# Optimization experiments

Measured on AMD Instinct MI355X. Metric: run time of the kernel, lower is better.

Reference implementation:

```python
import jax, jax.numpy as jnp
import numpy as np

N = 50000      # num_nodes
E = 800000     # num_edges
D = 128        # node feature dim
ED = 64        # edge feature dim
H = 4          # num_heads
U = 32         # units per head (units*heads == 128)


def setup_inputs() -> dict:
    key = jax.random.key(0)
    ks = jax.random.split(key, 12)
    inputs = jax.random.normal(ks[0], (N, D), dtype=jnp.float32)
    # tf.math.segment_* requires sorted segment ids -> sort source row
    src = jnp.sort(jax.random.randint(ks[1], (E,), 0, N, dtype=jnp.int32))
    dst = jax.random.randint(ks[2], (E,), 0, N, dtype=jnp.int32)
    edge_index = jnp.stack([src, dst], axis=0)
    edge_features = jax.random.normal(ks[3], (E, ED), dtype=jnp.float32)
    def glorot(k, shape):
        lim = np.sqrt(6.0 / (shape[0] + shape[1]))
        return jax.random.uniform(k, shape, jnp.float32, -lim, lim)
    HU = H * U
    return {
        "inputs": inputs,
        "edge_index": edge_index,
        "edge_features": edge_features,
        "Wq": glorot(ks[4], (D, HU)), "bq": jnp.zeros((HU,), jnp.float32),
        "Wk": glorot(ks[5], (D, HU)), "bk": jnp.zeros((HU,), jnp.float32),
        "Wv": glorot(ks[6], (D, HU)), "bv": jnp.zeros((HU,), jnp.float32),
        "We": glorot(ks[7], (ED, HU)), "be": jnp.zeros((HU,), jnp.float32),
        "Wo": glorot(ks[8], (HU, U)), "bo": jnp.zeros((U,), jnp.float32),
    }


def _segment_softmax(scores, seg, num_segments):
    # numerically stable segmented softmax over ragged neighborhoods
    seg_max = jax.ops.segment_max(scores, seg, num_segments=num_segments)
    ex = jnp.exp(scores - seg_max[seg])
    seg_sum = jax.ops.segment_sum(ex, seg, num_segments=num_segments)
    return ex / seg_sum[seg]


def reference(inputs, edge_index, edge_features, Wq, bq, Wk, bk, Wv, bv, We, be, Wo, bo):
    n = inputs.shape[0]
    q = (inputs @ Wq + bq).reshape(n, H, U)
    k = (inputs @ Wk + bk).reshape(n, H, U)
    v = (inputs @ Wv + bv).reshape(n, H, U)
    src, dst = edge_index[0], edge_index[1]
    qi = q[src]                      # [E, H, U]
    kj = k[dst]                      # [E, H, U]
    scores = jnp.sum(qi * kj, axis=-1)   # [E, H]
    eh = (edge_features @ We + be).reshape(-1, H, U)
    scores = scores + jnp.sum(eh * kj, axis=-1)
    attn = _segment_softmax(scores, src, n)        # [E, H]
    attended = jax.ops.segment_sum(attn[..., None] * v[dst], src, num_segments=n)
    attended = attended.reshape(n, H * U)
    return jax.nn.relu(attended @ Wo + bo)
```

## Files before the change

### kernel.cpp

```cpp
#include <hip/hip_runtime.h>
#include <math.h>

#define N_NODES 50000
#define N_EDGES 800000
#define D_IN    128
#define ED_IN   64
#define HU      128
#define NH      4
#define UD      32

#define NPB 16

typedef float fx4 __attribute__((ext_vector_type(4)));
typedef short s16x8 __attribute__((ext_vector_type(8)));
typedef float f32x4 __attribute__((ext_vector_type(4)));

static __device__ __forceinline__ unsigned short f2bf(float f) {
  unsigned u = __float_as_uint(f);
  unsigned r = (u + 0x7FFFu + ((u >> 16) & 1u)) >> 16;
  return (unsigned short)r;
}
static __device__ __forceinline__ float bf_lo(unsigned u) {
  return __uint_as_float(u << 16);
}
static __device__ __forceinline__ float bf_hi(unsigned u) {
  return __uint_as_float(u & 0xFFFF0000u);
}
static __device__ __forceinline__ float dot8(float4 a0, float4 a1, uint4 kk) {
  return a0.x * bf_lo(kk.x) + a0.y * bf_hi(kk.x)
       + a0.z * bf_lo(kk.y) + a0.w * bf_hi(kk.y)
       + a1.x * bf_lo(kk.z) + a1.y * bf_hi(kk.z)
       + a1.z * bf_lo(kk.w) + a1.w * bf_hi(kk.w);
}
static __device__ __forceinline__ float4 f4add(float4 a, float4 b) {
  return make_float4(a.x + b.x, a.y + b.y, a.z + b.z, a.w + b.w);
}

__global__ __launch_bounds__(256) void offsets_kernel(
    const int* __restrict__ src, int* __restrict__ off) {
  const int e = blockIdx.x * 256 + threadIdx.x;
  if (e >= N_EDGES) return;
  const int s = src[e];
  const int prev = (e == 0) ? -1 : src[e - 1];
  for (int n = prev + 1; n <= s; ++n) off[n] = e;
  if (e == N_EDGES - 1)
    for (int n = s + 1; n <= N_NODES; ++n) off[n] = N_EDGES;
}

__global__ __launch_bounds__(256) void wepack_kernel(
    const float* __restrict__ We, unsigned short* __restrict__ wf) {
  const int fl = blockIdx.x * 256 + threadIdx.x;
  if (fl >= 16 * 64) return;
  const int f = fl >> 6, lane = fl & 63;
  const int nt = f >> 1, kh = f & 1;
  const int n = nt * 16 + (lane & 15);
  const int kbase = kh * 32 + (lane >> 4) * 8;
#pragma unroll
  for (int j = 0; j < 8; ++j)
    wf[fl * 8 + j] = f2bf(We[(kbase + j) * HU + n]);
}

__global__ __launch_bounds__(128) void qkv_kernel(
    const float* __restrict__ x,
    const float* __restrict__ Wq, const float* __restrict__ bq,
    const float* __restrict__ Wk, const float* __restrict__ bk,
    const float* __restrict__ Wv, const float* __restrict__ bv,
    const float* __restrict__ be,
    float* __restrict__ q, unsigned short* __restrict__ kbf,
    unsigned short* __restrict__ vbf) {
  const int base = blockIdx.x * NPB;
  const int t = threadIdx.x;
  __shared__ float xs[NPB][D_IN];
  for (int j = 0; j < NPB; ++j)
    xs[j][t] = x[(long)(base + j) * D_IN + t];
  __syncthreads();
  float aq[NPB], ak[NPB], av[NPB];
  const float bqt = bq[t] + be[t], bkt = bk[t], bvt = bv[t];
#pragma unroll
  for (int j = 0; j < NPB; ++j) { aq[j] = bqt; ak[j] = bkt; av[j] = bvt; }
  for (int i = 0; i < D_IN; ++i) {
    const float wq = Wq[i * HU + t];
    const float wk = Wk[i * HU + t];
    const float wv = Wv[i * HU + t];
#pragma unroll
    for (int j = 0; j < NPB; ++j) {
      const float xi = xs[j][i];
      aq[j] += xi * wq; ak[j] += xi * wk; av[j] += xi * wv;
    }
  }
#pragma unroll
  for (int j = 0; j < NPB; ++j) {
    const long nn = base + j;
    q[nn * HU + t] = aq[j];
    kbf[nn * HU + t] = f2bf(ak[j]);
    vbf[nn * HU + t] = f2bf(av[j]);
  }
}

__global__ __launch_bounds__(256, 2) void score_kernel(
    const float* __restrict__ ef,
    const int* __restrict__ src, const int* __restrict__ dst,
    const float* __restrict__ q, const uint4* __restrict__ kbf,
    const s16x8* __restrict__ wf,
    float* __restrict__ scores) {
  __shared__ __align__(16) float ehs[64 * 128];
  const int t = threadIdx.x;
  const int w = t >> 6, l = t & 63;
  const long ebase = (long)blockIdx.x * 64;
  const int e = (int)(ebase + (t >> 2));
  const int h = t & 3;
  const int s = src[e], d = dst[e];

  const uint4* kp = kbf + (long)d * 16 + h * 4;
  const uint4 k0 = kp[0], k1 = kp[1], k2 = kp[2], k3 = kp[3];

  const float4* qp = (const float4*)(q + (long)s * HU + h * 32);
  const float4 q0 = qp[0], q1 = qp[1], q2 = qp[2], q3 = qp[3];
  const float4 q4 = qp[4], q5 = qp[5], q6 = qp[6], q7 = qp[7];

  const int arow = (int)(ebase + w * 16 + (l & 15));
  const fx4* ap = (const fx4*)(ef + (long)arow * ED_IN + (l >> 4) * 8);
  const fx4 a00 = __builtin_nontemporal_load(ap);
  const fx4 a01 = __builtin_nontemporal_load(ap + 1);
  const fx4 a10 = __builtin_nontemporal_load(ap + 8);
  const fx4 a11 = __builtin_nontemporal_load(ap + 9);
  s16x8 A0, A1;
  A0[0] = (short)f2bf(a00[0]); A0[1] = (short)f2bf(a00[1]);
  A0[2] = (short)f2bf(a00[2]); A0[3] = (short)f2bf(a00[3]);
  A0[4] = (short)f2bf(a01[0]); A0[5] = (short)f2bf(a01[1]);
  A0[6] = (short)f2bf(a01[2]); A0[7] = (short)f2bf(a01[3]);
  A1[0] = (short)f2bf(a10[0]); A1[1] = (short)f2bf(a10[1]);
  A1[2] = (short)f2bf(a10[2]); A1[3] = (short)f2bf(a10[3]);
  A1[4] = (short)f2bf(a11[0]); A1[5] = (short)f2bf(a11[1]);
  A1[6] = (short)f2bf(a11[2]); A1[7] = (short)f2bf(a11[3]);

  f32x4 acc[8];
#pragma unroll
  for (int nt = 0; nt < 8; ++nt) acc[nt] = (f32x4){0.f, 0.f, 0.f, 0.f};
#pragma unroll
  for (int nt = 0; nt < 8; ++nt) {
    const s16x8 B0 = wf[(nt * 2 + 0) * 64 + l];
    const s16x8 B1 = wf[(nt * 2 + 1) * 64 + l];
    acc[nt] = __builtin_amdgcn_mfma_f32_16x16x32_bf16(A0, B0, acc[nt], 0, 0, 0);
    acc[nt] = __builtin_amdgcn_mfma_f32_16x16x32_bf16(A1, B1, acc[nt], 0, 0, 0);
  }

  {
    const int nb = l & 15;
    const int mb = w * 16 + (l >> 4) * 4;
#pragma unroll
    for (int nt = 0; nt < 8; ++nt) {
#pragma unroll
      for (int r = 0; r < 4; ++r) {
        const int m = mb + r;
        const int b = (nt * 16 + nb) * 4;
        ehs[(m * 512 + (b ^ ((m & 7) << 4))) >> 2] = acc[nt][r];
      }
    }
  }
  asm volatile("s_waitcnt lgkmcnt(0)" ::: "memory");
  __builtin_amdgcn_sched_barrier(0);

  const int er = t >> 2;
  const int swz = (er & 7) << 4;
  const char* ehp = (const char*)ehs + er * 512;
#define EHV(i) (*(const float4*)(ehp + (((h * 128) + (i) * 16) ^ swz)))
  const float4 e0 = EHV(0), e1 = EHV(1), e2 = EHV(2), e3 = EHV(3);
  const float4 e4 = EHV(4), e5 = EHV(5), e6 = EHV(6), e7 = EHV(7);
#undef EHV
  const float p = dot8(f4add(q0, e0), f4add(q1, e1), k0)
                + dot8(f4add(q2, e2), f4add(q3, e3), k1)
                + dot8(f4add(q4, e4), f4add(q5, e5), k2)
                + dot8(f4add(q6, e6), f4add(q7, e7), k3);
  __builtin_nontemporal_store(p, scores + (long)e * NH + h);
}

__global__ __launch_bounds__(256) void aggregate_kernel(
    const int* __restrict__ off, const int* __restrict__ dst,
    const float* __restrict__ scores, const unsigned* __restrict__ v2,
    const float* __restrict__ Wo, const float* __restrict__ bo,
    float* __restrict__ out) {
  const int wv = threadIdx.x >> 6, l = threadIdx.x & 63;
  const int n = blockIdx.x * 4 + wv;
  const int h = l >> 4, q16 = l & 15;
  __shared__ float att[4][HU];

  const int start = off[n], end = off[n + 1];
  float m = -INFINITY, lsum = 0.f, a0 = 0.f, a1 = 0.f;
  for (int cs = start; cs < end; cs += 16) {
    const int e = cs + q16;
    const bool live = (e < end);
    const float sc = live ? __builtin_nontemporal_load(scores + (long)e * NH + h)
                          : -INFINITY;
    const int dl = live ? dst[e] : 0;
    float mc = sc;
#pragma unroll
    for (int o = 8; o > 0; o >>= 1) mc = fmaxf(mc, __shfl_xor(mc, o, 16));
    const float nm = fmaxf(m, mc);
    const float corr = __expf(m - nm);
    const float w = __expf(sc - nm);
    float ws = w;
#pragma unroll
    for (int o = 8; o > 0; o >>= 1) ws += __shfl_xor(ws, o, 16);
    lsum = lsum * corr + ws;
    a0 *= corr; a1 *= corr; m = nm;
#pragma unroll
    for (int j = 0; j < 16; ++j) {
      const float wj = __shfl(w, (l & 48) + j, 64);
      const int dj = __shfl(dl, (l & 48) + j, 64);
      const unsigned vr = v2[(long)dj * 64 + l];
      a0 += wj * bf_lo(vr);
      a1 += wj * bf_hi(vr);
    }
  }
  const float inv = (lsum > 0.f) ? 1.f / lsum : 0.f;
  att[wv][2 * l] = a0 * inv;
  att[wv][2 * l + 1] = a1 * inv;
  const int o = l & 31, half = l >> 5;
  float po = 0.f;
#pragma unroll
  for (int f = 0; f < 64; ++f)
    po += att[wv][half * 64 + f] * Wo[(half * 64 + f) * UD + o];
  po += __shfl_down(po, 32, 64);
  if (l < 32) out[(long)n * UD + l] = fmaxf(po + bo[l], 0.f);
}

extern "C" void kernel_launch(void* const* d_in, const int* in_sizes, int n_in,
                              void* d_out, int out_size, void* d_ws, size_t ws_size,
                              hipStream_t stream) {
  const float* x  = (const float*)d_in[0];
  const int*   ei = (const int*)d_in[1];
  const float* ef = (const float*)d_in[2];
  const float* Wq = (const float*)d_in[3];
  const float* bq = (const float*)d_in[4];
  const float* Wk = (const float*)d_in[5];
  const float* bk = (const float*)d_in[6];
  const float* Wv = (const float*)d_in[7];
  const float* bv = (const float*)d_in[8];
  const float* We = (const float*)d_in[9];
  const float* be = (const float*)d_in[10];
  const float* Wo = (const float*)d_in[11];
  const float* bo = (const float*)d_in[12];
  float* out = (float*)d_out;

  const int* src = ei;
  const int* dst = ei + N_EDGES;

  float* q = (float*)d_ws;
  unsigned short* kbf = (unsigned short*)(q + (long)N_NODES * HU);
  unsigned short* vbf = kbf + (long)N_NODES * HU;
  float* scores = (float*)(vbf + (long)N_NODES * HU);
  int* off = (int*)(scores + (long)N_EDGES * NH);
  unsigned short* wf = (unsigned short*)(((uintptr_t)(off + N_NODES + 1) + 15)
                                         & ~(uintptr_t)15);

  offsets_kernel<<<(N_EDGES + 255) / 256, 256, 0, stream>>>(src, off);
  wepack_kernel<<<4, 256, 0, stream>>>(We, wf);
  qkv_kernel<<<N_NODES / NPB, 128, 0, stream>>>(x, Wq, bq, Wk, bk, Wv, bv, be,
                                                q, kbf, vbf);
  score_kernel<<<N_EDGES / 64, 256, 0, stream>>>(ef, src, dst, q,
                                                 (const uint4*)kbf,
                                                 (const s16x8*)wf, scores);
  aggregate_kernel<<<N_NODES / 4, 256, 0, stream>>>(off, dst, scores,
                                                    (const unsigned*)vbf, Wo, bo, out);
}
```

Measured before the change: 513.4 us.

## Split score kernel into per-wave two-phase MFMA with halved LDS and registers

Restructures the score kernel so each wave works only on its own 16 edges. It computes the edge projection in two phases of 4 MFMA tiles, stores each phase in a per-wave LDS slice, and consumes it before the next phase. Each thread now handles half a head's dot product and combines the halves with a lane shuffle. This cuts LDS usage and live accumulator and q/k registers to raise occupancy, and the launch-bounds minimum is dropped. The cost is extra shuffles, duplicated q/k address computation across phases, and more waitcnt barriers.

```diff
diff --git a/kernel.cpp b/kernel.cpp
--- a/kernel.cpp
+++ b/kernel.cpp
@@ -97,26 +97,18 @@
   }
 }
 
-__global__ __launch_bounds__(256, 2) void score_kernel(
+__global__ __launch_bounds__(256) void score_kernel(
     const float* __restrict__ ef,
     const int* __restrict__ src, const int* __restrict__ dst,
-    const float* __restrict__ q, const uint4* __restrict__ kbf,
+    const float* __restrict__ q, const unsigned short* __restrict__ kbf,
     const s16x8* __restrict__ wf,
     float* __restrict__ scores) {
-  __shared__ __align__(16) float ehs[64 * 128];
+  __shared__ __align__(16) float ehs[4][16 * 64];
   const int t = threadIdx.x;
   const int w = t >> 6, l = t & 63;
   const long ebase = (long)blockIdx.x * 64;
-  const int e = (int)(ebase + (t >> 2));
-  const int h = t & 3;
+  const int e = (int)(ebase + w * 16 + (l >> 2));
   const int s = src[e], d = dst[e];
-
-  const uint4* kp = kbf + (long)d * 16 + h * 4;
-  const uint4 k0 = kp[0], k1 = kp[1], k2 = kp[2], k3 = kp[3];
-
-  const float4* qp = (const float4*)(q + (long)s * HU + h * 32);
-  const float4 q0 = qp[0], q1 = qp[1], q2 = qp[2], q3 = qp[3];
-  const float4 q4 = qp[4], q5 = qp[5], q6 = qp[6], q7 = qp[7];
 
   const int arow = (int)(ebase + w * 16 + (l & 15));
   const fx4* ap = (const fx4*)(ef + (long)arow * ED_IN + (l >> 4) * 8);
@@ -134,45 +126,60 @@
   A1[4] = (short)f2bf(a11[0]); A1[5] = (short)f2bf(a11[1]);
   A1[6] = (short)f2bf(a11[2]); A1[7] = (short)f2bf(a11[3]);
 
-  f32x4 acc[8];
-#pragma unroll
-  for (int nt = 0; nt < 8; ++nt) acc[nt] = (f32x4){0.f, 0.f, 0.f, 0.f};
-#pragma unroll
-  for (int nt = 0; nt < 8; ++nt) {
-    const s16x8 B0 = wf[(nt * 2 + 0) * 64 + l];
-    const s16x8 B1 = wf[(nt * 2 + 1) * 64 + l];
-    acc[nt] = __builtin_amdgcn_mfma_f32_16x16x32_bf16(A0, B0, acc[nt], 0, 0, 0);
-    acc[nt] = __builtin_amdgcn_mfma_f32_16x16x32_bf16(A1, B1, acc[nt], 0, 0, 0);
-  }
-
-  {
-    const int nb = l & 15;
-    const int mb = w * 16 + (l >> 4) * 4;
-#pragma unroll
-    for (int nt = 0; nt < 8; ++nt) {
+  float* __restrict__ ehw = ehs[w];
+  const int nb = l & 15, gbase = (l >> 4) * 4;
+  const int rloc = l >> 2;
+  const int hl = (l >> 1) & 1, half = l & 1;
+  const int swzr = (rloc & 7) << 4;
+
+#pragma unroll
+  for (int ph = 0; ph < 2; ++ph) {
+    f32x4 acc[4];
+#pragma unroll
+    for (int ntl = 0; ntl < 4; ++ntl) acc[ntl] = (f32x4){0.f, 0.f, 0.f, 0.f};
+#pragma unroll
+    for (int ntl = 0; ntl < 4; ++ntl) {
+      const int f = (ph * 4 + ntl) * 2;
+      const s16x8 B0 = wf[(f + 0) * 64 + l];
+      const s16x8 B1 = wf[(f + 1) * 64 + l];
+      acc[ntl] = __builtin_amdgcn_mfma_f32_16x16x32_bf16(A0, B0, acc[ntl], 0, 0, 0);
+      acc[ntl] = __builtin_amdgcn_mfma_f32_16x16x32_bf16(A1, B1, acc[ntl], 0, 0, 0);
+    }
+
+#pragma unroll
+    for (int ntl = 0; ntl < 4; ++ntl) {
 #pragma unroll
       for (int r = 0; r < 4; ++r) {
-        const int m = mb + r;
-        const int b = (nt * 16 + nb) * 4;
-        ehs[(m * 512 + (b ^ ((m & 7) << 4))) >> 2] = acc[nt][r];
+        const int m = gbase + r;
+        const int b = (ntl * 16 + nb) * 4;
+        ehw[(m * 256 + (b ^ ((m & 7) << 4))) >> 2] = acc[ntl][r];
       }
     }
-  }
-  asm volatile("s_waitcnt lgkmcnt(0)" ::: "memory");
-  __builtin_amdgcn_sched_barrier(0);
-
-  const int er = t >> 2;
-  const int swz = (er & 7) << 4;
-  const char* ehp = (const char*)ehs + er * 512;
-#define EHV(i) (*(const float4*)(ehp + (((h * 128) + (i) * 16) ^ swz)))
-  const float4 e0 = EHV(0), e1 = EHV(1), e2 = EHV(2), e3 = EHV(3);
-  const float4 e4 = EHV(4), e5 = EHV(5), e6 = EHV(6), e7 = EHV(7);
-#undef EHV
-  const float p = dot8(f4add(q0, e0), f4add(q1, e1), k0)
-                + dot8(f4add(q2, e2), f4add(q3, e3), k1)
-                + dot8(f4add(q4, e4), f4add(q5, e5), k2)
-                + dot8(f4add(q6, e6), f4add(q7, e7), k3);
-  __builtin_nontemporal_store(p, scores + (long)e * NH + h);
+    asm volatile("s_waitcnt lgkmcnt(0)" ::: "memory");
+    __builtin_amdgcn_sched_barrier(0);
+
+    const int h = ph * 2 + hl;
+    const char* ehp = (const char*)(ehw + rloc * 64);
+    const int cb = (l & 3) * 64;
+    const float4 e0 = *(const float4*)(ehp + ((cb + 0)  ^ swzr));
+    const float4 e1 = *(const float4*)(ehp + ((cb + 16) ^ swzr));
+    const float4 e2 = *(const float4*)(ehp + ((cb + 32) ^ swzr));
+    const float4 e3 = *(const float4*)(ehp + ((cb + 48) ^ swzr));
+
+    const float4* qp = (const float4*)(q + (long)s * HU + h * 32 + half * 16);
+    const float4 q0 = qp[0], q1 = qp[1], q2 = qp[2], q3 = qp[3];
+    const uint4* kp = (const uint4*)((const char*)kbf + (long)d * 256 + h * 64 + half * 32);
+    const uint4 k0 = kp[0], k1 = kp[1];
+
+    float p = dot8(f4add(q0, e0), f4add(q1, e1), k0)
+            + dot8(f4add(q2, e2), f4add(q3, e3), k1);
+    p += __shfl_xor(p, 1, 64);
+    if (!half)
+      __builtin_nontemporal_store(p, scores + (long)e * NH + h);
+
+    asm volatile("s_waitcnt lgkmcnt(0)" ::: "memory");
+    __builtin_amdgcn_sched_barrier(0);
+  }
 }
 
 __global__ __launch_bounds__(256) void aggregate_kernel(
@@ -258,8 +265,7 @@
   wepack_kernel<<<4, 256, 0, stream>>>(We, wf);
   qkv_kernel<<<N_NODES / NPB, 128, 0, stream>>>(x, Wq, bq, Wk, bk, Wv, bv, be,
                                                 q, kbf, vbf);
-  score_kernel<<<N_EDGES / 64, 256, 0, stream>>>(ef, src, dst, q,
-                                                 (const uint4*)kbf,
+  score_kernel<<<N_EDGES / 64, 256, 0, stream>>>(ef, src, dst, q, kbf,
                                                  (const s16x8*)wf, scores);
   aggregate_kernel<<<N_NODES / 4, 256, 0, stream>>>(off, dst, scores,
                                                     (const unsigned*)vbf, Wo, bo, out);
```

Result: faster. 493.6 us (-3.9%).
